# Kernel tuning notes

Measured on AMD Instinct MI355X. Metric: run time of the kernel, lower is better.

The kernel has to match this reference:

```python
import jax, jax.numpy as jnp
import numpy as np
from jax import lax

B, T, L = 256, 512, 128


def setup_inputs() -> dict:
    key = jax.random.key(0)
    k1, k2, k3 = jax.random.split(key, 3)
    labels = jax.random.randint(k1, (B, T), 0, L)
    y_true = jax.nn.one_hot(labels, L, dtype=jnp.float32)  # [B,T,L]
    y_pred = jax.random.normal(k2, (B, T, L), dtype=jnp.float32)
    trans = jax.random.normal(k3, (L, L), dtype=jnp.float32) * 0.1
    return {"y_true": y_true, "y_pred": y_pred, "trans": trans}


def reference(y_true, y_pred, trans):
    # ---- log partition via forward algorithm (lax.scan over time) ----
    init = y_pred[:, 0]  # [B,L] initial alpha

    def step(alpha, emit):  # alpha [B,L], emit [B,L]
        # alpha[:, i, None] + trans[i, j] -> logsumexp over previous label i
        new = jax.nn.logsumexp(alpha[:, :, None] + trans[None, :, :], axis=1) + emit
        return new, None

    emits = jnp.swapaxes(y_pred[:, 1:], 0, 1)  # [T-1,B,L]
    final_alpha, _ = lax.scan(step, init, emits)  # [B,L]
    log_norm = jax.nn.logsumexp(final_alpha, axis=1, keepdims=True)  # [B,1]

    # ---- path score (unnormalized log prob of the true path) ----
    point_score = jnp.sum(y_pred * y_true, axis=(1, 2), keepdims=False)[:, None]  # [B,1]
    trans_score = jnp.einsum('bti,btj,ij->b', y_true[:, :-1], y_true[:, 1:], trans)[:, None]  # [B,1]

    return log_norm - (point_score + trans_score)  # [B,1]
```

## Files before the change

kernel.cpp:

```cpp
#include <hip/hip_runtime.h>

typedef float    f32x4  __attribute__((ext_vector_type(4)));
typedef short    s16x8  __attribute__((ext_vector_type(8)));
typedef unsigned uivec2 __attribute__((ext_vector_type(2)));
typedef unsigned uivec4 __attribute__((ext_vector_type(4)));

#define Tt 512
#define Ll 128
#define CH 32
#define CL 16
#define NR 31
#define NRECB 248

#define WS_PTP 0
#define WS_KR  2048
#define WS_KB  (2048 + 256*NR)
#define WS_RV  (2048 + 2*256*NR)
#define WS_BV  (WS_RV + 256*NR*128)
#define WS_END (WS_BV + 256*NR*128)
#define WS_LAB_BYTES ((size_t)WS_END * 4)

__device__ __forceinline__ ushort bf16rn(float f) {
  unsigned u = __float_as_uint(f);
  u += 0x7FFFu + ((u >> 16) & 1u);
  return (ushort)(u >> 16);
}
__device__ __forceinline__ unsigned cvtpk(float a, float b) {
  unsigned d;
  asm("v_cvt_pk_bf16_f32 %0, %1, %2" : "=v"(d) : "v"(a), "v"(b));
  return d;
}
__device__ __forceinline__ float4 expf4(float4 v) {
  float4 r; r.x = __expf(v.x); r.y = __expf(v.y); r.z = __expf(v.z); r.w = __expf(v.w);
  return r;
}
__device__ __forceinline__ float4 mul4(float4 v, float s) {
  v.x *= s; v.y *= s; v.z *= s; v.w *= s; return v;
}

__global__ __attribute__((amdgpu_flat_work_group_size(256, 256),
                          amdgpu_waves_per_eu(1)))
void crf_rec(const float* __restrict__ yp_g, const float* __restrict__ tr_g,
             float* __restrict__ wsf)
{
  __shared__ __align__(16) char smem[32768];
  const int tid = threadIdx.x, wv = tid >> 6, l = tid & 63;

  const int task = blockIdx.x * 4 + wv;
  const bool FWD = task < 496;
  int g, c;
  if (FWD) { g = task / 31; c = task % 31; }
  else     { int t2 = task - 496; g = t2 / 31; c = t2 % 31 + 1; }
  const int b0  = g * 16;
  const int l15 = l & 15, q = l >> 4;
  const int t_hi = (c == CH - 1) ? (Tt - 1) : (c * CL + CL);
  const int t_lo = c * CL + 1;
  const int n    = FWD ? CL : (t_hi - t_lo + 1);

  s16x8 Bf[8][4];
  if (FWD) {
    #pragma unroll
    for (int kt = 0; kt < 4; ++kt)
      #pragma unroll
      for (int e = 0; e < 8; ++e) {
        const int jin = 32 * kt + 16 * (e >> 2) + 4 * q + (e & 3);
        const float* rp_ = tr_g + jin * Ll + l15;
        #pragma unroll
        for (int tl = 0; tl < 8; ++tl)
          Bf[tl][kt][e] = (short)bf16rn(__expf(rp_[16 * tl]));
      }
  } else {
    #pragma unroll
    for (int tl = 0; tl < 8; ++tl) {
      const float* rp_ = tr_g + (l15 + 16 * tl) * Ll + 4 * q;
      #pragma unroll
      for (int kt = 0; kt < 4; ++kt)
        #pragma unroll
        for (int r = 0; r < 2; ++r) {
          float4 tv = *(const float4*)(rp_ + 32 * kt + 16 * r);
          Bf[tl][kt][4 * r + 0] = (short)bf16rn(__expf(tv.x));
          Bf[tl][kt][4 * r + 1] = (short)bf16rn(__expf(tv.y));
          Bf[tl][kt][4 * r + 2] = (short)bf16rn(__expf(tv.z));
          Bf[tl][kt][4 * r + 3] = (short)bf16rn(__expf(tv.w));
        }
    }
  }

  const unsigned sbase = (unsigned)(size_t)(&smem[0]);
  const unsigned wvoff = (unsigned)(wv * 8192);
  const unsigned lane8 = (unsigned)(l * 8);
  const int wroff = wv * 8192 + l15 * 32 + q * 8;
  const float* emb = yp_g + (size_t)(b0 + l15) * (Tt * Ll) + 4 * q;
  float Kacc = 0.f;

#define LOADSLOT(S, TAU)                                                      \
  { const float* ep_ = emb + (size_t)(TAU) * Ll;                              \
    S##0 = *(const float4*)(ep_ + 0);   S##1 = *(const float4*)(ep_ + 16);    \
    S##2 = *(const float4*)(ep_ + 32);  S##3 = *(const float4*)(ep_ + 48);    \
    S##4 = *(const float4*)(ep_ + 64);  S##5 = *(const float4*)(ep_ + 80);    \
    S##6 = *(const float4*)(ep_ + 96);  S##7 = *(const float4*)(ep_ + 112); }

#define TRREAD8(RBUF, T0,T1,T2,T3,T4,T5,T6,T7)                                \
  { unsigned ra_ = sbase + wvoff + (unsigned)((RBUF) * 4096) + lane8;         \
    asm volatile(                                                             \
      "ds_read_b64_tr_b16 %0, %8 offset:0\n\t"                                \
      "ds_read_b64_tr_b16 %1, %8 offset:512\n\t"                              \
      "ds_read_b64_tr_b16 %2, %8 offset:1024\n\t"                             \
      "ds_read_b64_tr_b16 %3, %8 offset:1536\n\t"                             \
      "ds_read_b64_tr_b16 %4, %8 offset:2048\n\t"                             \
      "ds_read_b64_tr_b16 %5, %8 offset:2560\n\t"                             \
      "ds_read_b64_tr_b16 %6, %8 offset:3072\n\t"                             \
      "ds_read_b64_tr_b16 %7, %8 offset:3584\n\t"                             \
      "s_waitcnt lgkmcnt(0)"                                                  \
      : "=v"(T0), "=v"(T1), "=v"(T2), "=v"(T3),                               \
        "=v"(T4), "=v"(T5), "=v"(T6), "=v"(T7)                                \
      : "v"(ra_) : "memory"); }

#define BUILDA(A_, TA, TB, WA, WB_)                                           \
  { uivec4 au_;                                                               \
    au_.x = cvtpk(__uint_as_float(TA.x << 16) * WA.x,                         \
                  __uint_as_float(TA.x & 0xFFFF0000u) * WA.y);                \
    au_.y = cvtpk(__uint_as_float(TA.y << 16) * WA.z,                         \
                  __uint_as_float(TA.y & 0xFFFF0000u) * WA.w);                \
    au_.z = cvtpk(__uint_as_float(TB.x << 16) * WB_.x,                        \
                  __uint_as_float(TB.x & 0xFFFF0000u) * WB_.y);               \
    au_.w = cvtpk(__uint_as_float(TB.y << 16) * WB_.z,                        \
                  __uint_as_float(TB.y & 0xFFFF0000u) * WB_.w);               \
    A_ = __builtin_bit_cast(s16x8, au_); }

#define MFMAW(WBUF)                                                           \
  { f32x4 dd[8];                                                              \
    _Pragma("unroll")                                                         \
    for (int tl = 0; tl < 8; ++tl) {                                          \
      f32x4 z = {0.f, 0.f, 0.f, 0.f};                                         \
      z = __builtin_amdgcn_mfma_f32_16x16x32_bf16(A0, Bf[tl][0], z, 0, 0, 0); \
      z = __builtin_amdgcn_mfma_f32_16x16x32_bf16(A1, Bf[tl][1], z, 0, 0, 0); \
      z = __builtin_amdgcn_mfma_f32_16x16x32_bf16(A2, Bf[tl][2], z, 0, 0, 0); \
      z = __builtin_amdgcn_mfma_f32_16x16x32_bf16(A3, Bf[tl][3], z, 0, 0, 0); \
      dd[tl] = z;                                                             \
    }                                                                         \
    _Pragma("unroll")                                                         \
    for (int tl = 0; tl < 8; ++tl) {                                          \
      uivec2 w_;                                                              \
      w_.x = cvtpk(dd[tl][0], dd[tl][1]);                                     \
      w_.y = cvtpk(dd[tl][2], dd[tl][3]);                                     \
      *(uivec2*)(smem + wroff + (WBUF) * 4096 + tl * 512) = w_;               \
    } }

#define MULT(RBUF, WBUF, S, REN, PT, PSLOT)                                   \
  { asm volatile("s_waitcnt lgkmcnt(0)" ::: "memory");                        \
    uivec2 t0, t1, t2, t3, t4, t5, t6, t7;                                    \
    TRREAD8(RBUF, t0, t1, t2, t3, t4, t5, t6, t7)                             \
    float4 we0 = expf4(S##0), we1 = expf4(S##1), we2 = expf4(S##2),           \
           we3 = expf4(S##3), we4 = expf4(S##4), we5 = expf4(S##5),           \
           we6 = expf4(S##6), we7 = expf4(S##7);                              \
    if (REN) {                                                                \
      float pf = __uint_as_float(__builtin_amdgcn_readfirstlane(t0.x << 16)); \
      Kacc += __logf(pf);                                                     \
      float rs = __builtin_amdgcn_rcpf(pf);                                   \
      we0 = mul4(we0, rs); we1 = mul4(we1, rs); we2 = mul4(we2, rs);          \
      we3 = mul4(we3, rs); we4 = mul4(we4, rs); we5 = mul4(we5, rs);          \
      we6 = mul4(we6, rs); we7 = mul4(we7, rs);                               \
    }                                                                         \
    s16x8 A0, A1, A2, A3;                                                     \
    BUILDA(A0, t0, t1, we0, we1)                                              \
    BUILDA(A1, t2, t3, we2, we3)                                              \
    BUILDA(A2, t4, t5, we4, we5)                                              \
    BUILDA(A3, t6, t7, we6, we7)                                              \
    MFMAW(WBUF)                                                               \
    if ((PT) >= 0) LOADSLOT(PSLOT, PT) }

  float4 SA0, SA1, SA2, SA3, SA4, SA5, SA6, SA7;
  float4 SB0, SB1, SB2, SB3, SB4, SB5, SB6, SB7;
  const int tau1 = FWD ? (t_lo - 1) : t_hi;
  const int tau2 = FWD ? t_lo : (t_hi - 1);
  LOADSLOT(SB, tau1)
  LOADSLOT(SA, tau2)

  {
    s16x8 A0, A1, A2, A3;
    if (FWD && c > 0) {
      uivec4 au; au.x = au.y = au.z = au.w = 0x3F803F80u;
      A0 = __builtin_bit_cast(s16x8, au); A1 = A0; A2 = A0; A3 = A0;
    } else {
      float4 we0 = expf4(SB0), we1 = expf4(SB1), we2 = expf4(SB2),
             we3 = expf4(SB3), we4 = expf4(SB4), we5 = expf4(SB5),
             we6 = expf4(SB6), we7 = expf4(SB7);
      uivec4 a0; a0.x = cvtpk(we0.x, we0.y); a0.y = cvtpk(we0.z, we0.w);
      a0.z = cvtpk(we1.x, we1.y); a0.w = cvtpk(we1.z, we1.w);
      uivec4 a1; a1.x = cvtpk(we2.x, we2.y); a1.y = cvtpk(we2.z, we2.w);
      a1.z = cvtpk(we3.x, we3.y); a1.w = cvtpk(we3.z, we3.w);
      uivec4 a2; a2.x = cvtpk(we4.x, we4.y); a2.y = cvtpk(we4.z, we4.w);
      a2.z = cvtpk(we5.x, we5.y); a2.w = cvtpk(we5.z, we5.w);
      uivec4 a3; a3.x = cvtpk(we6.x, we6.y); a3.y = cvtpk(we6.z, we6.w);
      a3.z = cvtpk(we7.x, we7.y); a3.w = cvtpk(we7.z, we7.w);
      A0 = __builtin_bit_cast(s16x8, a0); A1 = __builtin_bit_cast(s16x8, a1);
      A2 = __builtin_bit_cast(s16x8, a2); A3 = __builtin_bit_cast(s16x8, a3);
    }
    MFMAW(1)
    const int tau3 = FWD ? (t_lo + 1) : (t_hi - 2);
    LOADSLOT(SB, tau3)
  }

  for (int k = 2; k + 1 <= n; k += 2) {
    const int ta = FWD ? (t_lo + k) : (t_hi - k - 1);
    MULT(1, 0, SA, false, ta, SA)
    const bool ren = ((k + 1) == 9) || ((k + 1) == 15);
    const int tb = (k + 3 <= n + 1) ? (FWD ? (t_lo + k + 1) : (t_hi - k - 2))
                                    : -1;
    MULT(0, 1, SB, ren, tb, SB)
  }
  if ((n & 1) == 0) {
    MULT(1, 0, SA, false, -1, SA)
  }

  {
    asm volatile("s_waitcnt lgkmcnt(0)" ::: "memory");
    uivec2 t0, t1, t2, t3, t4, t5, t6, t7;
    TRREAD8((n & 1), t0, t1, t2, t3, t4, t5, t6, t7)
    float4 wf0, wf1, wf2, wf3, wf4, wf5, wf6, wf7;
    if (FWD) {
      wf0 = expf4(SB0); wf1 = expf4(SB1); wf2 = expf4(SB2); wf3 = expf4(SB3);
      wf4 = expf4(SB4); wf5 = expf4(SB5); wf6 = expf4(SB6); wf7 = expf4(SB7);
    } else {
      float4 one = {1.f, 1.f, 1.f, 1.f};
      wf0 = wf1 = wf2 = wf3 = wf4 = wf5 = wf6 = wf7 = one;
    }
    const int cs = FWD ? c : (c - 1);
    float* rp0 = wsf + (FWD ? WS_RV : WS_BV)
               + ((size_t)(b0 + l15) * NR + cs) * 128 + 4 * q;
#define STOREV(I, T_, W_)                                                     \
    { float4 o_;                                                              \
      o_.x = __uint_as_float(T_.x << 16) * W_.x;                              \
      o_.y = __uint_as_float(T_.x & 0xFFFF0000u) * W_.y;                      \
      o_.z = __uint_as_float(T_.y << 16) * W_.z;                              \
      o_.w = __uint_as_float(T_.y & 0xFFFF0000u) * W_.w;                      \
      *(float4*)(rp0 + 16 * (I)) = o_; }
    STOREV(0, t0, wf0) STOREV(1, t1, wf1) STOREV(2, t2, wf2) STOREV(3, t3, wf3)
    STOREV(4, t4, wf4) STOREV(5, t5, wf5) STOREV(6, t6, wf6) STOREV(7, t7, wf7)
#undef STOREV
    if (q == 0) {
      float* kp = wsf + (FWD ? WS_KR : WS_KB);
      kp[(b0 + l15) * NR + cs] = Kacc;
    }
  }
#undef MULT
#undef MFMAW
#undef BUILDA
#undef TRREAD8
#undef LOADSLOT
}

__global__ __launch_bounds__(256) void crf_score(
    const float* __restrict__ yt_g, const float* __restrict__ yp_g,
    float* __restrict__ wsf, unsigned char* __restrict__ lab_g)
{
  __shared__ float red[4];
  const int bid = blockIdx.x;
  const int b = bid >> 3, seg = bid & 7;
  const int tid = threadIdx.x, wv = tid >> 6, l = tid & 63;
  const float4* yp4 = (const float4*)(yp_g + ((size_t)b * Tt + seg * 64) * Ll);
  const float4* yt4 = (const float4*)(yt_g + ((size_t)b * Tt + seg * 64) * Ll);
  unsigned char* lb = lab_g + b * Tt + seg * 64;
  float pt = 0.f;
  #pragma unroll
  for (int i = 0; i < 8; ++i) {
    int f = tid + i * 256;
    float4 a = yp4[f], y = yt4[f];
    pt += a.x * y.x + a.y * y.y + a.z * y.z + a.w * y.w;
    int t = f >> 5, jb = (f & 31) << 2;
    if (y.x > .5f) lb[t] = (unsigned char)jb;
    if (y.y > .5f) lb[t] = (unsigned char)(jb + 1);
    if (y.z > .5f) lb[t] = (unsigned char)(jb + 2);
    if (y.w > .5f) lb[t] = (unsigned char)(jb + 3);
  }
  #pragma unroll
  for (int o = 32; o; o >>= 1) pt += __shfl_xor(pt, o);
  if (l == 0) red[wv] = pt;
  __syncthreads();
  if (tid == 0) wsf[WS_PTP + b * 8 + seg] = red[0] + red[1] + red[2] + red[3];
}

__global__ __launch_bounds__(64) void crf_stitch(
    const float* __restrict__ wsf, const unsigned char* __restrict__ lab_g,
    const float* __restrict__ tr_g, float* __restrict__ out)
{
  const int b = blockIdx.x, j = threadIdx.x;
  const float* RV = wsf + WS_RV + (size_t)b * NR * 128;
  const float* BV = wsf + WS_BV + (size_t)b * NR * 128;
  const float* Kr = wsf + WS_KR + b * NR;
  const float* Kb = wsf + WS_KB + b * NR;
  float lz;
  {
    float d = RV[j] * BV[j] + RV[j + 64] * BV[j + 64];
    #pragma unroll
    for (int o = 32; o; o >>= 1) d += __shfl_xor(d, o);
    lz = __logf(d) + Kr[0] + Kb[0];
  }
  #pragma unroll
  for (int cc = 1; cc < NR; ++cc) {
    float d = RV[cc*128 + j] * BV[cc*128 + j] + RV[cc*128 + j + 64] * BV[cc*128 + j + 64];
    float s = RV[cc*128 + j] + RV[cc*128 + j + 64];
    #pragma unroll
    for (int o = 32; o; o >>= 1) { d += __shfl_xor(d, o); s += __shfl_xor(s, o); }
    lz += __logf(d) - __logf(s) + Kb[cc];
  }
  const unsigned char* lb = lab_g + b * Tt;
  float tp = (j < 8) ? wsf[WS_PTP + b * 8 + j] : 0.f;
  #pragma unroll
  for (int i = 0; i < 8; ++i) {
    int t = j + i * 64;
    if (t < Tt - 1) tp += tr_g[(int)lb[t] * Ll + (int)lb[t + 1]];
  }
  #pragma unroll
  for (int o = 32; o; o >>= 1) tp += __shfl_xor(tp, o);
  if (j == 0) out[b] = lz - tp;
}

extern "C" void kernel_launch(void* const* d_in, const int* in_sizes, int n_in,
                              void* d_out, int out_size, void* d_ws, size_t ws_size,
                              hipStream_t stream) {
  const float* y_true = (const float*)d_in[0];
  const float* y_pred = (const float*)d_in[1];
  const float* trans  = (const float*)d_in[2];
  float* out = (float*)d_out;
  float* wsf = (float*)d_ws;
  unsigned char* lab = (unsigned char*)d_ws + WS_LAB_BYTES;
  crf_rec  <<<dim3(NRECB), dim3(256), 0, stream>>>(y_pred, trans, wsf);
  crf_score<<<dim3(2048),  dim3(256), 0, stream>>>(y_true, y_pred, wsf, lab);
  crf_stitch<<<dim3(256),  dim3(64),  0, stream>>>(wsf, lab, trans, out);
}
```

Measured before the change: 66.96 us.

## Halve chunk length to 8 steps and store chunk vectors as bf16

Splits the time axis into 64 chunks of 8 steps instead of 32 of 16, doubling the number of independent recurrence tasks (2016 waves, 504 blocks). This shortens each wave's serial chain and fills more CUs. The per-chunk boundary vectors are now stored as bf16 instead of fp32, which offsets the doubled workspace traffic. The renormalisation point and the workspace offsets are adjusted to match. The costs are a serial stitch loop twice as long, no longer unrolled, and lower precision in the stitched partition sums.

```diff
diff --git a/kernel.cpp b/kernel.cpp
--- a/kernel.cpp
+++ b/kernel.cpp
@@ -7,24 +7,27 @@
 
 #define Tt 512
 #define Ll 128
-#define CH 32
-#define CL 16
-#define NR 31
-#define NRECB 248
-
-#define WS_PTP 0
-#define WS_KR  2048
-#define WS_KB  (2048 + 256*NR)
-#define WS_RV  (2048 + 2*256*NR)
-#define WS_BV  (WS_RV + 256*NR*128)
-#define WS_END (WS_BV + 256*NR*128)
-#define WS_LAB_BYTES ((size_t)WS_END * 4)
+#define CH 64
+#define CL 8
+#define NR 63
+#define NTASK 2016
+#define NRECB 504
+
+#define WSB_PTP 0
+#define WSB_KR  8192
+#define WSB_KB  72704
+#define WSB_RV  137216
+#define WSB_BV  4265984
+#define WSB_LAB 8394752
 
 __device__ __forceinline__ ushort bf16rn(float f) {
   unsigned u = __float_as_uint(f);
   u += 0x7FFFu + ((u >> 16) & 1u);
   return (ushort)(u >> 16);
 }
+__device__ __forceinline__ float bf16tof(ushort h) {
+  return __uint_as_float(((unsigned)h) << 16);
+}
 __device__ __forceinline__ unsigned cvtpk(float a, float b) {
   unsigned d;
   asm("v_cvt_pk_bf16_f32 %0, %1, %2" : "=v"(d) : "v"(a), "v"(b));
@@ -41,16 +44,16 @@
 __global__ __attribute__((amdgpu_flat_work_group_size(256, 256),
                           amdgpu_waves_per_eu(1)))
 void crf_rec(const float* __restrict__ yp_g, const float* __restrict__ tr_g,
-             float* __restrict__ wsf)
+             char* __restrict__ wsb)
 {
   __shared__ __align__(16) char smem[32768];
   const int tid = threadIdx.x, wv = tid >> 6, l = tid & 63;
 
   const int task = blockIdx.x * 4 + wv;
-  const bool FWD = task < 496;
+  const bool FWD = task < (16 * NR);
   int g, c;
-  if (FWD) { g = task / 31; c = task % 31; }
-  else     { int t2 = task - 496; g = t2 / 31; c = t2 % 31 + 1; }
+  if (FWD) { g = task / NR; c = task % NR; }
+  else     { int t2 = task - 16 * NR; g = t2 / NR; c = t2 % NR + 1; }
   const int b0  = g * 16;
   const int l15 = l & 15, q = l >> 4;
   const int t_hi = (c == CH - 1) ? (Tt - 1) : (c * CL + CL);
@@ -205,7 +208,7 @@
   for (int k = 2; k + 1 <= n; k += 2) {
     const int ta = FWD ? (t_lo + k) : (t_hi - k - 1);
     MULT(1, 0, SA, false, ta, SA)
-    const bool ren = ((k + 1) == 9) || ((k + 1) == 15);
+    const bool ren = ((k + 1) == 5);
     const int tb = (k + 3 <= n + 1) ? (FWD ? (t_lo + k + 1) : (t_hi - k - 2))
                                     : -1;
     MULT(0, 1, SB, ren, tb, SB)
@@ -227,20 +230,20 @@
       wf0 = wf1 = wf2 = wf3 = wf4 = wf5 = wf6 = wf7 = one;
     }
     const int cs = FWD ? c : (c - 1);
-    float* rp0 = wsf + (FWD ? WS_RV : WS_BV)
-               + ((size_t)(b0 + l15) * NR + cs) * 128 + 4 * q;
+    ushort* rp0 = (ushort*)(wsb + (FWD ? WSB_RV : WSB_BV))
+                + ((size_t)(b0 + l15) * NR + cs) * 128 + 4 * q;
 #define STOREV(I, T_, W_)                                                     \
-    { float4 o_;                                                              \
-      o_.x = __uint_as_float(T_.x << 16) * W_.x;                              \
-      o_.y = __uint_as_float(T_.x & 0xFFFF0000u) * W_.y;                      \
-      o_.z = __uint_as_float(T_.y << 16) * W_.z;                              \
-      o_.w = __uint_as_float(T_.y & 0xFFFF0000u) * W_.w;                      \
-      *(float4*)(rp0 + 16 * (I)) = o_; }
+    { uivec2 h_;                                                              \
+      h_.x = cvtpk(__uint_as_float(T_.x << 16) * W_.x,                        \
+                   __uint_as_float(T_.x & 0xFFFF0000u) * W_.y);               \
+      h_.y = cvtpk(__uint_as_float(T_.y << 16) * W_.z,                        \
+                   __uint_as_float(T_.y & 0xFFFF0000u) * W_.w);               \
+      *(uivec2*)(rp0 + 16 * (I)) = h_; }
     STOREV(0, t0, wf0) STOREV(1, t1, wf1) STOREV(2, t2, wf2) STOREV(3, t3, wf3)
     STOREV(4, t4, wf4) STOREV(5, t5, wf5) STOREV(6, t6, wf6) STOREV(7, t7, wf7)
 #undef STOREV
     if (q == 0) {
-      float* kp = wsf + (FWD ? WS_KR : WS_KB);
+      float* kp = (float*)(wsb + (FWD ? WSB_KR : WSB_KB));
       kp[(b0 + l15) * NR + cs] = Kacc;
     }
   }
@@ -278,35 +281,37 @@
   for (int o = 32; o; o >>= 1) pt += __shfl_xor(pt, o);
   if (l == 0) red[wv] = pt;
   __syncthreads();
-  if (tid == 0) wsf[WS_PTP + b * 8 + seg] = red[0] + red[1] + red[2] + red[3];
+  if (tid == 0) wsf[b * 8 + seg] = red[0] + red[1] + red[2] + red[3];
 }
 
 __global__ __launch_bounds__(64) void crf_stitch(
-    const float* __restrict__ wsf, const unsigned char* __restrict__ lab_g,
-    const float* __restrict__ tr_g, float* __restrict__ out)
+    const char* __restrict__ wsb, const float* __restrict__ tr_g,
+    float* __restrict__ out)
 {
   const int b = blockIdx.x, j = threadIdx.x;
-  const float* RV = wsf + WS_RV + (size_t)b * NR * 128;
-  const float* BV = wsf + WS_BV + (size_t)b * NR * 128;
-  const float* Kr = wsf + WS_KR + b * NR;
-  const float* Kb = wsf + WS_KB + b * NR;
+  const float*  wsf = (const float*)wsb;
+  const ushort* RV  = (const ushort*)(wsb + WSB_RV) + (size_t)b * NR * 128;
+  const ushort* BV  = (const ushort*)(wsb + WSB_BV) + (size_t)b * NR * 128;
+  const float*  Kr  = (const float*)(wsb + WSB_KR) + b * NR;
+  const float*  Kb  = (const float*)(wsb + WSB_KB) + b * NR;
   float lz;
   {
-    float d = RV[j] * BV[j] + RV[j + 64] * BV[j + 64];
+    float d = bf16tof(RV[j]) * bf16tof(BV[j])
+            + bf16tof(RV[j + 64]) * bf16tof(BV[j + 64]);
     #pragma unroll
     for (int o = 32; o; o >>= 1) d += __shfl_xor(d, o);
     lz = __logf(d) + Kr[0] + Kb[0];
   }
-  #pragma unroll
   for (int cc = 1; cc < NR; ++cc) {
-    float d = RV[cc*128 + j] * BV[cc*128 + j] + RV[cc*128 + j + 64] * BV[cc*128 + j + 64];
-    float s = RV[cc*128 + j] + RV[cc*128 + j + 64];
+    float r0 = bf16tof(RV[cc * 128 + j]), r1 = bf16tof(RV[cc * 128 + j + 64]);
+    float d = r0 * bf16tof(BV[cc * 128 + j]) + r1 * bf16tof(BV[cc * 128 + j + 64]);
+    float s = r0 + r1;
     #pragma unroll
     for (int o = 32; o; o >>= 1) { d += __shfl_xor(d, o); s += __shfl_xor(s, o); }
     lz += __logf(d) - __logf(s) + Kb[cc];
   }
-  const unsigned char* lb = lab_g + b * Tt;
-  float tp = (j < 8) ? wsf[WS_PTP + b * 8 + j] : 0.f;
+  const unsigned char* lb = (const unsigned char*)(wsb + WSB_LAB) + b * Tt;
+  float tp = (j < 8) ? wsf[b * 8 + j] : 0.f;
   #pragma unroll
   for (int i = 0; i < 8; ++i) {
     int t = j + i * 64;
@@ -324,9 +329,10 @@
   const float* y_pred = (const float*)d_in[1];
   const float* trans  = (const float*)d_in[2];
   float* out = (float*)d_out;
-  float* wsf = (float*)d_ws;
-  unsigned char* lab = (unsigned char*)d_ws + WS_LAB_BYTES;
-  crf_rec  <<<dim3(NRECB), dim3(256), 0, stream>>>(y_pred, trans, wsf);
-  crf_score<<<dim3(2048),  dim3(256), 0, stream>>>(y_true, y_pred, wsf, lab);
-  crf_stitch<<<dim3(256),  dim3(64),  0, stream>>>(wsf, lab, trans, out);
-}
+  char*  wsb = (char*)d_ws;
+  crf_rec   <<<dim3(NRECB), dim3(256), 0, stream>>>(y_pred, trans, wsb);
+  crf_score <<<dim3(2048),  dim3(256), 0, stream>>>(y_true, y_pred,
+                                                    (float*)wsb,
+                                                    (unsigned char*)(wsb + WSB_LAB));
+  crf_stitch<<<dim3(256),   dim3(64),  0, stream>>>(wsb, trans, out);
+}
```

Result: slower. 104.0 us (+55.4%).
